# Performance work log

Measured on AMD Instinct MI355X. Metric: run time of the kernel, lower is better.

## Reference

```python
import jax, jax.numpy as jnp
import numpy as np

IN_NC = 32
OUT_NC = 32
HIDDEN = 192  # in_nc * expand_ratio(6)
KS = 3
EPS = 1e-5


def setup_inputs() -> dict:
    key = jax.random.key(0)
    k1, k2 = jax.random.split(key)
    b, h, w = 8, 128, 128
    fh = fw = 8
    hyper = IN_NC * HIDDEN + HIDDEN * KS * KS + HIDDEN * OUT_NC  # 14016
    return {
        "x": jax.random.normal(k1, (b, IN_NC, h, w), jnp.float32),
        "s": jax.random.normal(k2, (b, hyper, fh, fw), jnp.float32),
        "g1": jnp.ones((HIDDEN,), jnp.float32),
        "b1": jnp.zeros((HIDDEN,), jnp.float32),
        "g2": jnp.ones((HIDDEN,), jnp.float32),
        "b2": jnp.zeros((HIDDEN,), jnp.float32),
        "g3": jnp.ones((OUT_NC,), jnp.float32),
        "b3": jnp.zeros((OUT_NC,), jnp.float32),
    }


def _bn(x, gamma, beta):
    # x: [P, H, W, C]; training-mode BatchNorm2d over (P, H, W) per channel
    mean = jnp.mean(x, axis=(0, 1, 2))
    var = jnp.var(x, axis=(0, 1, 2))  # biased, matches torch normalization
    return (x - mean) * jax.lax.rsqrt(var + EPS) * gamma + beta


def _relu6(x):
    return jnp.clip(x, 0.0, 6.0)


def _forward(x, s, g1, b1, g2, b2, g3, b3):
    b, c, h, w = x.shape
    fh, fw = s.shape[-2], s.shape[-1]
    ph, pw = h // fh, w // fw
    kh, kw = ph + 2, pw + 2  # padding (1,1)

    # reflect-pad then unfold into per-patch tiles [P, kh, kw, c]
    xp = jnp.pad(x, ((0, 0), (0, 0), (1, 1), (1, 1)), mode="reflect")
    xp = xp.transpose(0, 2, 3, 1)  # [b, h+2, w+2, c]
    ih = jnp.arange(fh)[:, None] * ph + jnp.arange(kh)[None, :]  # [fh, kh]
    iw = jnp.arange(fw)[:, None] * pw + jnp.arange(kw)[None, :]  # [fw, kw]
    t = xp[:, ih]            # [b, fh, kh, w+2, c]
    t = t[:, :, :, iw]       # [b, fh, kh, fw, kw, c]
    patches = t.transpose(0, 1, 3, 2, 4, 5).reshape(b * fh * fw, kh, kw, c)

    # per-patch hypernet weights
    wt = s.transpose(0, 2, 3, 1).reshape(b * fh * fw, -1)  # [P, hyper]
    r1 = IN_NC * HIDDEN
    r2 = r1 + HIDDEN * KS * KS
    w1 = wt[:, :r1].reshape(-1, HIDDEN, IN_NC)          # pointwise expand
    w2 = wt[:, r1:r2].reshape(-1, HIDDEN, KS, KS)        # depthwise 3x3
    w3 = wt[:, r2:].reshape(-1, OUT_NC, HIDDEN)          # pointwise project

    # 1x1 expand + BN + ReLU6
    x1 = jnp.einsum("pijc,poc->pijo", patches, w1)       # [P, kh, kw, hidden]
    x1 = _relu6(_bn(x1, g1, b1))

    # depthwise 3x3 (valid, stride 1) + BN + ReLU6
    ii = jnp.arange(ph)[:, None] + jnp.arange(KS)[None, :]
    jj = jnp.arange(pw)[:, None] + jnp.arange(KS)[None, :]
    win = x1[:, ii]          # [P, ph, 3, kw, hidden]
    win = win[:, :, :, jj]   # [P, ph, 3, pw, 3, hidden]
    x2 = jnp.einsum("piujvc,pcuv->pijc", win, w2)        # [P, ph, pw, hidden]
    x2 = _relu6(_bn(x2, g2, b2))

    # 1x1 project + BN
    x3 = jnp.einsum("pijc,poc->pijo", x2, w3)            # [P, ph, pw, out]
    x3 = _bn(x3, g3, b3)

    out = x3.reshape(b, fh, fw, ph, pw, OUT_NC)
    out = out.transpose(0, 5, 1, 3, 2, 4).reshape(b, OUT_NC, h, w)
    return x + out  # use_res_connect: stride==1 and in_nc==out_nc


def reference(x, s, g1, b1, g2, b2, g3, b3):
    return _forward(x, s, g1, b1, g2, b2, g3, b3)
```

## Files before the change

kernel.cpp:

```cpp
#include <hip/hip_runtime.h>

#define EPS 1e-5f

namespace {
constexpr int HYPER = 14016;
constexpr int HID   = 192;
constexpr int A1    = 324;
constexpr int A2    = 256;
constexpr int P_TOT = 512;
constexpr int W1SZ  = 6144;
constexpr int WT2SZ = 7872;
constexpr int R3OFF = 1728;

constexpr size_t WB1_B = 0;
constexpr size_t WT2_B = 6291456;
constexpr size_t X2_B  = WT2_B + 16121856;
constexpr size_t X3_B  = X2_B + 50331648;
constexpr size_t SUM_B = X3_B + 16777216;
}

typedef __attribute__((ext_vector_type(8))) short bf16x8;
typedef __attribute__((ext_vector_type(4))) float f32x4;

__device__ __forceinline__ float relu6f(float v) { return fminf(fmaxf(v, 0.f), 6.f); }

__device__ __forceinline__ float bf2f(unsigned int h) {
  return __uint_as_float(h << 16);
}
__device__ __forceinline__ unsigned short f2bf(float f) {
  unsigned int u = __float_as_uint(f);
  return (unsigned short)((u + 0x7FFFu + ((u >> 16) & 1u)) >> 16);
}

__device__ __host__ __forceinline__ int afrag_slot(int o, int c) {
  return (o >> 4) * 512 + (c >> 3) * 128 + (o & 15) * 8 + (c & 7);
}

__global__ __launch_bounds__(256) void k0_transpose(const float* __restrict__ s,
                                                    unsigned short* __restrict__ wb1,
                                                    float* __restrict__ wt2) {
  __shared__ float tile[64][65];
  const int blk = blockIdx.x;
  const int b  = blk / 219;
  const int kt = blk - b * 219;
  const int k0 = kt * 64;
  const int t  = threadIdx.x;
  {
    const int f  = t & 63;
    const int kr = t >> 6;
    const float* sp = s + ((size_t)b * HYPER + k0 + kr) * 64 + f;
#pragma unroll
    for (int kk = 0; kk < 16; kk++)
      tile[kr + kk * 4][f] = sp[(size_t)kk * 4 * 64];
  }
  __syncthreads();
  {
    const int kk = t & 63;
    const int fr = t >> 6;
    if (kt < 96) {
      const int k = k0 + kk;
      const int o = k >> 5, c = k & 31;
      const int slot = afrag_slot(o, c);
      unsigned short* wp = wb1 + ((size_t)b * 64 + fr) * W1SZ + slot;
#pragma unroll
      for (int ff = 0; ff < 16; ff++)
        wp[(size_t)ff * 4 * W1SZ] = f2bf(tile[kk][fr + ff * 4]);
    } else {
      float* wp = wt2 + ((size_t)b * 64 + fr) * WT2SZ + (k0 - W1SZ) + kk;
#pragma unroll
      for (int ff = 0; ff < 16; ff++)
        wp[(size_t)ff * 4 * WT2SZ] = tile[kk][fr + ff * 4];
    }
  }
}

__global__ __launch_bounds__(256) void k1_stats(const float* __restrict__ x,
                                                const unsigned short* __restrict__ wb1,
                                                float* __restrict__ sums) {
  __shared__ __align__(16) unsigned short pL[21 * 512];
  __shared__ float stat[384];
  const int p  = blockIdx.x;
  const int b  = p >> 6;
  const int fi = (p >> 3) & 7;
  const int fj = p & 7;
  const int t  = threadIdx.x;

  for (int i = t; i < 384; i += 256) stat[i] = 0.f;

  const int row0 = fi * 16 - 1, col0 = fj * 16 - 1;
  const float* xb = x + (size_t)b * 32 * 128 * 128;
  for (int idx = t; idx < 32 * A1; idx += 256) {
    int c  = idx / A1;
    int ij = idx - c * A1;
    int ii = ij / 18;
    int jj = ij - ii * 18;
    int r  = row0 + ii; r  = (r  < 0) ? 1 : (r  > 127) ? 126 : r;
    int cl = col0 + jj; cl = (cl < 0) ? 1 : (cl > 127) ? 126 : cl;
    int slot = ((ij >> 4) * 4 + (c >> 3)) * 128 + (ij & 15) * 8 + (c & 7);
    pL[slot] = f2bf(xb[((size_t)c * 128 + r) * 128 + cl]);
  }
  __syncthreads();

  const int lane = t & 63;
  const int wv   = t >> 6;
  const int m16  = lane & 15;
  const int quad = lane >> 4;
  const unsigned short* wbp = wb1 + (size_t)p * W1SZ;

  for (int oi = 0; oi < 3; oi++) {
    const int ot = wv + oi * 4;
    bf16x8 a = *(const bf16x8*)(wbp + ot * 512 + lane * 8);
    float sacc[4] = {0.f, 0.f, 0.f, 0.f};
    float qacc[4] = {0.f, 0.f, 0.f, 0.f};
    for (int jt = 0; jt < 21; jt++) {
      bf16x8 bb = *(const bf16x8*)&pL[jt * 512 + lane * 8];
      f32x4 d = __builtin_amdgcn_mfma_f32_16x16x32_bf16(a, bb, (f32x4){0.f, 0.f, 0.f, 0.f}, 0, 0, 0);
      const int ij = jt * 16 + m16;
      if (ij < A1) {
#pragma unroll
        for (int r = 0; r < 4; r++) {
          float v = d[r];
          sacc[r] += v;
          qacc[r] = fmaf(v, v, qacc[r]);
        }
      }
    }
#pragma unroll
    for (int r = 0; r < 4; r++) {
      float sv = sacc[r], qv = qacc[r];
#pragma unroll
      for (int msk = 1; msk < 16; msk <<= 1) {
        sv += __shfl_xor(sv, msk, 64);
        qv += __shfl_xor(qv, msk, 64);
      }
      if (m16 == 0) {
        int o = ot * 16 + quad * 4 + r;
        atomicAdd(&stat[o], sv);
        atomicAdd(&stat[192 + o], qv);
      }
    }
  }
  __syncthreads();
  for (int i = t; i < 384; i += 256) atomicAdd(&sums[i], stat[i]);
}

__global__ __launch_bounds__(256) void k2_fused(const float* __restrict__ x,
                                                const unsigned short* __restrict__ wb1,
                                                const float* __restrict__ wt2,
                                                const float* __restrict__ sums,
                                                const float* __restrict__ g1,
                                                const float* __restrict__ b1,
                                                unsigned short* __restrict__ x2,
                                                float* __restrict__ sums2) {
  __shared__ __align__(16) unsigned short pL[21 * 512];
  __shared__ __align__(16) unsigned short xc[2][324 * 18];
  __shared__ __align__(16) unsigned short x2s[256 * 18];
  __shared__ float sc[HID], sh[HID];
  __shared__ float st2[384];
  const int p  = blockIdx.x;
  const int b  = p >> 6;
  const int fi = (p >> 3) & 7;
  const int fj = p & 7;
  const int t  = threadIdx.x;

  const float inv1 = 1.f / 165888.f;
  for (int c = t; c < HID; c += 256) {
    float m   = sums[c] * inv1;
    float var = sums[192 + c] * inv1 - m * m;
    float scl = g1[c] * rsqrtf(var + EPS);
    sc[c] = scl;
    sh[c] = b1[c] - m * scl;
  }
  for (int i = t; i < 384; i += 256) st2[i] = 0.f;

  const int row0 = fi * 16 - 1, col0 = fj * 16 - 1;
  const float* xb = x + (size_t)b * 32 * 128 * 128;
  for (int idx = t; idx < 32 * A1; idx += 256) {
    int c  = idx / A1;
    int ij = idx - c * A1;
    int ii = ij / 18;
    int jj = ij - ii * 18;
    int r  = row0 + ii; r  = (r  < 0) ? 1 : (r  > 127) ? 126 : r;
    int cl = col0 + jj; cl = (cl < 0) ? 1 : (cl > 127) ? 126 : cl;
    int slot = ((ij >> 4) * 4 + (c >> 3)) * 128 + (ij & 15) * 8 + (c & 7);
    pL[slot] = f2bf(xb[((size_t)c * 128 + r) * 128 + cl]);
  }
  __syncthreads();

  const int lane = t & 63;
  const int wv   = t >> 6;
  const int m16  = lane & 15;
  const int quad = lane >> 4;
  const int cdw  = t >> 4;
  const int jdw  = t & 15;
  const float* w2p = wt2 + (size_t)p * WT2SZ;
  unsigned short* x2base = x2 + (size_t)p * 12 * 4096;
  const unsigned short* wbp = wb1 + (size_t)p * W1SZ;

  for (int ri = 0; ri < 6; ri++) {
    const int sub = wv & 1;
    const int ot  = ri * 2 + sub;
    const int jt0 = (wv >> 1) * 11;
    const int jt1 = jt0 + 11 - (wv >> 1);
    bf16x8 a = *(const bf16x8*)(wbp + ot * 512 + lane * 8);
    for (int jt = jt0; jt < jt1; jt++) {
      bf16x8 bb = *(const bf16x8*)&pL[jt * 512 + lane * 8];
      f32x4 d = __builtin_amdgcn_mfma_f32_16x16x32_bf16(a, bb, (f32x4){0.f, 0.f, 0.f, 0.f}, 0, 0, 0);
      const int ij = jt * 16 + m16;
      if (ij < A1) {
        unsigned short* xcp = &xc[sub][ij * 18 + quad * 4];
#pragma unroll
        for (int r = 0; r < 4; r++) {
          int ch = ot * 16 + quad * 4 + r;
          float v = relu6f(fmaf(d[r], sc[ch], sh[ch]));
          xcp[r] = f2bf(v);
        }
      }
    }
    __syncthreads();
    for (int sub2 = 0; sub2 < 2; sub2++) {
      const int ot2 = ri * 2 + sub2;
      const int ch  = ot2 * 16 + cdw;
      float wr[9];
#pragma unroll
      for (int u = 0; u < 9; u++) wr[u] = w2p[ch * 9 + u];
      float accs[16];
#pragma unroll
      for (int i = 0; i < 16; i++) accs[i] = 0.f;
      const unsigned short* xcs = &xc[sub2][0];
#pragma unroll
      for (int r = 0; r < 18; r++) {
        const unsigned short* bp = &xcs[(r * 18 + jdw) * 18 + cdw];
        float v0 = bf2f(bp[0]);
        float v1 = bf2f(bp[18]);
        float v2 = bf2f(bp[36]);
#pragma unroll
        for (int u = 0; u < 3; u++) {
          int i = r - u;
          if (i >= 0 && i < 16)
            accs[i] = fmaf(v0, wr[u * 3 + 0],
                      fmaf(v1, wr[u * 3 + 1],
                      fmaf(v2, wr[u * 3 + 2], accs[i])));
        }
      }
      float ls = 0.f, lq = 0.f;
#pragma unroll
      for (int i = 0; i < 16; i++) {
        unsigned short h = f2bf(accs[i]);
        float rv = bf2f(h);
        ls += rv;
        lq = fmaf(rv, rv, lq);
        x2s[(i * 16 + jdw) * 18 + cdw] = h;
      }
#pragma unroll
      for (int msk = 1; msk < 16; msk <<= 1) {
        ls += __shfl_xor(ls, msk, 64);
        lq += __shfl_xor(lq, msk, 64);
      }
      if (jdw == 0) {
        atomicAdd(&st2[ch], ls);
        atomicAdd(&st2[192 + ch], lq);
      }
      __syncthreads();
      unsigned short* dst = x2base + (size_t)ot2 * 4096;
#pragma unroll
      for (int k = 0; k < 4; k++) {
        int g  = (k * 256 + t) * 4;
        int ij = g >> 4, c0 = g & 15;
        unsigned int a0 = *(const unsigned int*)&x2s[ij * 18 + c0];
        unsigned int a1 = *(const unsigned int*)&x2s[ij * 18 + c0 + 2];
        uint2 v; v.x = a0; v.y = a1;
        *(uint2*)&dst[g] = v;
      }
      __syncthreads();
    }
  }
  for (int i = t; i < 384; i += 256) atomicAdd(&sums2[i], st2[i]);
}

__global__ __launch_bounds__(256) void k3_pw2(const unsigned short* __restrict__ x2,
                                              const float* __restrict__ wt2,
                                              const float* __restrict__ sums2,
                                              const float* __restrict__ g2,
                                              const float* __restrict__ b2,
                                              float* __restrict__ x3,
                                              float* __restrict__ sums3) {
  __shared__ __align__(16) unsigned short wA[12 * 512];
  __shared__ float sc[HID], sh[HID];
  __shared__ float st3[64];
  const int blk  = blockIdx.x;
  const int p    = blk >> 1;
  const int half = blk & 1;
  const int t    = threadIdx.x;
  const float inv = 1.f / 131072.f;
  for (int c = t; c < HID; c += 256) {
    float m   = sums2[c] * inv;
    float var = sums2[192 + c] * inv - m * m;
    float scl = g2[c] * rsqrtf(var + EPS);
    sc[c] = scl;
    sh[c] = b2[c] - m * scl;
  }
  if (t < 64) st3[t] = 0.f;
  const float* w3p = wt2 + (size_t)p * WT2SZ + R3OFF;
  for (int idx = t; idx < 32 * 48; idx += 256) {
    int o  = idx / 48;
    int c4 = idx - o * 48;
    float4 v = *(const float4*)&w3p[o * HID + c4 * 4];
    int slot = ((o >> 4) * 6 + (c4 >> 3)) * 512 + ((((c4 >> 1) & 3) * 16) + (o & 15)) * 8 + (c4 & 1) * 4;
    ushort4 u;
    u.x = f2bf(v.x); u.y = f2bf(v.y); u.z = f2bf(v.z); u.w = f2bf(v.w);
    *(ushort4*)&wA[slot] = u;
  }
  __syncthreads();
  const int lane = t & 63;
  const int wv   = t >> 6;
  const int m16  = lane & 15;
  const int kg   = lane >> 4;
  bf16x8 aF[2][6];
#pragma unroll
  for (int ot = 0; ot < 2; ot++)
#pragma unroll
    for (int ks = 0; ks < 6; ks++)
      aF[ot][ks] = *(const bf16x8*)&wA[(ot * 6 + ks) * 512 + lane * 8];
  const unsigned short* x2p = x2 + (size_t)p * 12 * 4096;
  f32x4 acc[2][2];
#pragma unroll
  for (int it = 0; it < 2; it++)
#pragma unroll
    for (int ot = 0; ot < 2; ot++)
#pragma unroll
      for (int r = 0; r < 4; r++) acc[it][ot][r] = 0.f;
#pragma unroll
  for (int it = 0; it < 2; it++) {
    const int ijt = half * 8 + wv + it * 4;
    const int ij  = ijt * 16 + m16;
    const unsigned short* brow = x2p + (size_t)(kg >> 1) * 4096 + (size_t)ij * 16 + (kg & 1) * 8;
#pragma unroll
    for (int ks = 0; ks < 6; ks++) {
      ushort4 u0 = *(const ushort4*)&brow[ks * 8192];
      ushort4 u1 = *(const ushort4*)&brow[ks * 8192 + 4];
      const float* scp = &sc[ks * 32 + kg * 8];
      const float* shp = &sh[ks * 32 + kg * 8];
      unsigned short uu[8] = {u0.x, u0.y, u0.z, u0.w, u1.x, u1.y, u1.z, u1.w};
      bf16x8 bb;
#pragma unroll
      for (int j = 0; j < 8; j++) {
        float y = relu6f(fmaf(bf2f(uu[j]), scp[j], shp[j]));
        bb[j] = (short)f2bf(y);
      }
      acc[it][0] = __builtin_amdgcn_mfma_f32_16x16x32_bf16(aF[0][ks], bb, acc[it][0], 0, 0, 0);
      acc[it][1] = __builtin_amdgcn_mfma_f32_16x16x32_bf16(aF[1][ks], bb, acc[it][1], 0, 0, 0);
    }
  }
  float* x3p = x3 + (size_t)p * 32 * A2;
  float sacc[2][4] = {{0.f}}, qacc[2][4] = {{0.f}};
#pragma unroll
  for (int it = 0; it < 2; it++) {
    const int ijt = half * 8 + wv + it * 4;
#pragma unroll
    for (int ot = 0; ot < 2; ot++) {
#pragma unroll
      for (int r = 0; r < 4; r++) {
        float v = acc[it][ot][r];
        x3p[(size_t)(ot * 16 + kg * 4 + r) * A2 + ijt * 16 + m16] = v;
        sacc[ot][r] += v;
        qacc[ot][r] = fmaf(v, v, qacc[ot][r]);
      }
    }
  }
#pragma unroll
  for (int ot = 0; ot < 2; ot++)
#pragma unroll
    for (int r = 0; r < 4; r++) {
      float sv = sacc[ot][r], qv = qacc[ot][r];
#pragma unroll
      for (int msk = 1; msk < 16; msk <<= 1) {
        sv += __shfl_xor(sv, msk, 64);
        qv += __shfl_xor(qv, msk, 64);
      }
      if (m16 == 0) {
        int o = ot * 16 + kg * 4 + r;
        atomicAdd(&st3[o], sv);
        atomicAdd(&st3[32 + o], qv);
      }
    }
  __syncthreads();
  if (t < 64) atomicAdd(&sums3[t], st3[t]);
}

__global__ __launch_bounds__(256) void k4_out(const float* __restrict__ x,
                                              const float* __restrict__ x3,
                                              const float* __restrict__ sums3,
                                              const float* __restrict__ g3,
                                              const float* __restrict__ b3,
                                              float* __restrict__ out) {
  const int idx4 = blockIdx.x * 256 + threadIdx.x;
  const int w4 = idx4 & 31;
  int tmp = idx4 >> 5;
  const int h = tmp & 127; tmp >>= 7;
  const int o = tmp & 31;
  const int b = tmp >> 5;
  const int fi = h >> 4, i = h & 15;
  const int fj = w4 >> 2;
  const int j0 = (w4 & 3) * 4;
  const int p   = b * 64 + fi * 8 + fj;
  const int ij0 = i * 16 + j0;
  const float inv = 1.f / 131072.f;
  float m   = sums3[o] * inv;
  float var = sums3[32 + o] * inv - m * m;
  float sv  = g3[o] * rsqrtf(var + EPS);
  float shv = b3[o] - m * sv;
  float4 xv = *(const float4*)&x[(size_t)idx4 * 4];
  float4 v  = *(const float4*)&x3[((size_t)p * 32 + o) * A2 + ij0];
  float4 r;
  r.x = fmaf(v.x, sv, shv) + xv.x;
  r.y = fmaf(v.y, sv, shv) + xv.y;
  r.z = fmaf(v.z, sv, shv) + xv.z;
  r.w = fmaf(v.w, sv, shv) + xv.w;
  *(float4*)&out[(size_t)idx4 * 4] = r;
}

extern "C" void kernel_launch(void* const* d_in, const int* in_sizes, int n_in,
                              void* d_out, int out_size, void* d_ws, size_t ws_size,
                              hipStream_t stream) {
  const float* x  = (const float*)d_in[0];
  const float* s  = (const float*)d_in[1];
  const float* g1 = (const float*)d_in[2];
  const float* b1 = (const float*)d_in[3];
  const float* g2 = (const float*)d_in[4];
  const float* b2 = (const float*)d_in[5];
  const float* g3 = (const float*)d_in[6];
  const float* b3 = (const float*)d_in[7];
  char* base = (char*)d_ws;
  unsigned short* wb1  = (unsigned short*)(base + WB1_B);
  float*          wt2  = (float*)(base + WT2_B);
  unsigned short* x2   = (unsigned short*)(base + X2_B);
  float*          x3   = (float*)(base + X3_B);
  float*          sums = (float*)(base + SUM_B);
  float* out = (float*)d_out;

  hipMemsetAsync(sums, 0, 832 * sizeof(float), stream);
  k0_transpose<<<8 * 219, 256, 0, stream>>>(s, wb1, wt2);
  k1_stats<<<P_TOT, 256, 0, stream>>>(x, wb1, sums);
  k2_fused<<<P_TOT, 256, 0, stream>>>(x, wb1, wt2, sums, g1, b1, x2, sums + 384);
  k3_pw2<<<1024, 256, 0, stream>>>(x2, wt2, sums + 384, g2, b2, x3, sums + 768);
  k4_out<<<4096, 256, 0, stream>>>(x, x3, sums + 768, g3, b3, out);
}
```

Measured before the change: 223.0 us.

## Restructure fused depthwise stage and store projection output as bf16

The fused expand+depthwise kernel now processes one 16-channel tile at a time. It interleaves the next tile's MFMA expand with the current tile's store, stages the depthwise weights in shared memory, and switches to a channel-major xc layout where each thread computes two adjacent columns over eight rows. The projection output x3 is stored as bf16 rather than fp32, which halves the intermediate traffic between k3 and k4, and the BN statistics are taken on the rounded values. This trades some accuracy in the final BN input for less memory traffic, and cuts the barriers per channel group in k2.

New measurement: 221.0 us. About the same (-0.9%).

```diff
diff --git a/kernel.cpp b/kernel.cpp
--- a/kernel.cpp
+++ b/kernel.cpp
@@ -16,7 +16,7 @@
 constexpr size_t WT2_B = 6291456;
 constexpr size_t X2_B  = WT2_B + 16121856;
 constexpr size_t X3_B  = X2_B + 50331648;
-constexpr size_t SUM_B = X3_B + 16777216;
+constexpr size_t SUM_B = X3_B + 8388608;
 }
 
 typedef __attribute__((ext_vector_type(8))) short bf16x8;
@@ -153,8 +153,9 @@
                                                 unsigned short* __restrict__ x2,
                                                 float* __restrict__ sums2) {
   __shared__ __align__(16) unsigned short pL[21 * 512];
-  __shared__ __align__(16) unsigned short xc[2][324 * 18];
+  __shared__ __align__(16) unsigned short xc[16 * 328];
   __shared__ __align__(16) unsigned short x2s[256 * 18];
+  __shared__ float w2L[HID * 9];
   __shared__ float sc[HID], sh[HID];
   __shared__ float st2[384];
   const int p  = blockIdx.x;
@@ -172,6 +173,10 @@
     sh[c] = b1[c] - m * scl;
   }
   for (int i = t; i < 384; i += 256) st2[i] = 0.f;
+  {
+    const float* wtp = wt2 + (size_t)p * WT2SZ;
+    for (int i = t; i < HID * 9; i += 256) w2L[i] = wtp[i];
+  }
 
   const int row0 = fi * 16 - 1, col0 = fj * 16 - 1;
   const float* xb = x + (size_t)b * 32 * 128 * 128;
@@ -191,89 +196,95 @@
   const int wv   = t >> 6;
   const int m16  = lane & 15;
   const int quad = lane >> 4;
-  const int cdw  = t >> 4;
-  const int jdw  = t & 15;
-  const float* w2p = wt2 + (size_t)p * WT2SZ;
+  const int ih  = t >> 7;
+  const int cdw = (t >> 3) & 15;
+  const int jp  = t & 7;
+  const unsigned short* wbp = wb1 + (size_t)p * W1SZ;
   unsigned short* x2base = x2 + (size_t)p * 12 * 4096;
-  const unsigned short* wbp = wb1 + (size_t)p * W1SZ;
-
-  for (int ri = 0; ri < 6; ri++) {
-    const int sub = wv & 1;
-    const int ot  = ri * 2 + sub;
-    const int jt0 = (wv >> 1) * 11;
-    const int jt1 = jt0 + 11 - (wv >> 1);
-    bf16x8 a = *(const bf16x8*)(wbp + ot * 512 + lane * 8);
-    for (int jt = jt0; jt < jt1; jt++) {
+
+  auto conv1 = [&](int rt) {
+    bf16x8 a = *(const bf16x8*)(wbp + rt * 512 + lane * 8);
+    for (int jt = wv; jt < 21; jt += 4) {
       bf16x8 bb = *(const bf16x8*)&pL[jt * 512 + lane * 8];
       f32x4 d = __builtin_amdgcn_mfma_f32_16x16x32_bf16(a, bb, (f32x4){0.f, 0.f, 0.f, 0.f}, 0, 0, 0);
       const int ij = jt * 16 + m16;
       if (ij < A1) {
-        unsigned short* xcp = &xc[sub][ij * 18 + quad * 4];
 #pragma unroll
         for (int r = 0; r < 4; r++) {
-          int ch = ot * 16 + quad * 4 + r;
+          int cl = quad * 4 + r;
+          int ch = rt * 16 + cl;
           float v = relu6f(fmaf(d[r], sc[ch], sh[ch]));
-          xcp[r] = f2bf(v);
+          xc[cl * 328 + ij] = f2bf(v);
         }
       }
     }
-    __syncthreads();
-    for (int sub2 = 0; sub2 < 2; sub2++) {
-      const int ot2 = ri * 2 + sub2;
-      const int ch  = ot2 * 16 + cdw;
+  };
+
+  conv1(0);
+  __syncthreads();
+
+  for (int rt = 0; rt < 12; rt++) {
+    {
+      const int ch = rt * 16 + cdw;
       float wr[9];
 #pragma unroll
-      for (int u = 0; u < 9; u++) wr[u] = w2p[ch * 9 + u];
-      float accs[16];
-#pragma unroll
-      for (int i = 0; i < 16; i++) accs[i] = 0.f;
-      const unsigned short* xcs = &xc[sub2][0];
-#pragma unroll
-      for (int r = 0; r < 18; r++) {
-        const unsigned short* bp = &xcs[(r * 18 + jdw) * 18 + cdw];
-        float v0 = bf2f(bp[0]);
-        float v1 = bf2f(bp[18]);
-        float v2 = bf2f(bp[36]);
+      for (int u = 0; u < 9; u++) wr[u] = w2L[ch * 9 + u];
+      float a0[8], a1[8];
+#pragma unroll
+      for (int i = 0; i < 8; i++) { a0[i] = 0.f; a1[i] = 0.f; }
+      const unsigned short* xcc = &xc[cdw * 328];
+#pragma unroll
+      for (int rr = 0; rr < 10; rr++) {
+        const int rg = ih * 8 + rr;
+        unsigned int d0 = *(const unsigned int*)&xcc[rg * 18 + jp * 2];
+        unsigned int d1 = *(const unsigned int*)&xcc[rg * 18 + jp * 2 + 2];
+        float v0 = bf2f(d0 & 0xFFFFu), v1 = bf2f(d0 >> 16);
+        float v2 = bf2f(d1 & 0xFFFFu), v3 = bf2f(d1 >> 16);
 #pragma unroll
         for (int u = 0; u < 3; u++) {
-          int i = r - u;
-          if (i >= 0 && i < 16)
-            accs[i] = fmaf(v0, wr[u * 3 + 0],
-                      fmaf(v1, wr[u * 3 + 1],
-                      fmaf(v2, wr[u * 3 + 2], accs[i])));
+          int il = rr - u;
+          if (il >= 0 && il < 8) {
+            a0[il] = fmaf(v0, wr[u * 3 + 0], fmaf(v1, wr[u * 3 + 1], fmaf(v2, wr[u * 3 + 2], a0[il])));
+            a1[il] = fmaf(v1, wr[u * 3 + 0], fmaf(v2, wr[u * 3 + 1], fmaf(v3, wr[u * 3 + 2], a1[il])));
+          }
         }
       }
       float ls = 0.f, lq = 0.f;
 #pragma unroll
-      for (int i = 0; i < 16; i++) {
-        unsigned short h = f2bf(accs[i]);
-        float rv = bf2f(h);
-        ls += rv;
-        lq = fmaf(rv, rv, lq);
-        x2s[(i * 16 + jdw) * 18 + cdw] = h;
-      }
-#pragma unroll
-      for (int msk = 1; msk < 16; msk <<= 1) {
-        ls += __shfl_xor(ls, msk, 64);
-        lq += __shfl_xor(lq, msk, 64);
-      }
-      if (jdw == 0) {
+      for (int il = 0; il < 8; il++) {
+        const int ig = ih * 8 + il;
+        const int j0 = jp * 2;
+        unsigned short h0 = f2bf(a0[il]);
+        unsigned short h1 = f2bf(a1[il]);
+        float r0 = bf2f(h0), r1 = bf2f(h1);
+        ls += r0 + r1;
+        lq = fmaf(r0, r0, fmaf(r1, r1, lq));
+        x2s[(ig * 16 + j0) * 18 + cdw]     = h0;
+        x2s[(ig * 16 + j0 + 1) * 18 + cdw] = h1;
+      }
+      ls += __shfl_xor(ls, 1, 64); lq += __shfl_xor(lq, 1, 64);
+      ls += __shfl_xor(ls, 2, 64); lq += __shfl_xor(lq, 2, 64);
+      ls += __shfl_xor(ls, 4, 64); lq += __shfl_xor(lq, 4, 64);
+      if (jp == 0) {
         atomicAdd(&st2[ch], ls);
         atomicAdd(&st2[192 + ch], lq);
       }
-      __syncthreads();
-      unsigned short* dst = x2base + (size_t)ot2 * 4096;
+    }
+    __syncthreads();
+    {
+      unsigned short* dst = x2base + (size_t)rt * 4096;
 #pragma unroll
       for (int k = 0; k < 4; k++) {
         int g  = (k * 256 + t) * 4;
         int ij = g >> 4, c0 = g & 15;
-        unsigned int a0 = *(const unsigned int*)&x2s[ij * 18 + c0];
-        unsigned int a1 = *(const unsigned int*)&x2s[ij * 18 + c0 + 2];
-        uint2 v; v.x = a0; v.y = a1;
+        unsigned int v0 = *(const unsigned int*)&x2s[ij * 18 + c0];
+        unsigned int v1 = *(const unsigned int*)&x2s[ij * 18 + c0 + 2];
+        uint2 v; v.x = v0; v.y = v1;
         *(uint2*)&dst[g] = v;
       }
-      __syncthreads();
-    }
+    }
+    if (rt < 11) conv1(rt + 1);
+    __syncthreads();
   }
   for (int i = t; i < 384; i += 256) atomicAdd(&sums2[i], st2[i]);
 }
@@ -283,7 +294,7 @@
                                               const float* __restrict__ sums2,
                                               const float* __restrict__ g2,
                                               const float* __restrict__ b2,
-                                              float* __restrict__ x3,
+                                              unsigned short* __restrict__ x3,
                                               float* __restrict__ sums3) {
   __shared__ __align__(16) unsigned short wA[12 * 512];
   __shared__ float sc[HID], sh[HID];
@@ -352,7 +363,7 @@
       acc[it][1] = __builtin_amdgcn_mfma_f32_16x16x32_bf16(aF[1][ks], bb, acc[it][1], 0, 0, 0);
     }
   }
-  float* x3p = x3 + (size_t)p * 32 * A2;
+  unsigned short* x3p = x3 + (size_t)p * 32 * A2;
   float sacc[2][4] = {{0.f}}, qacc[2][4] = {{0.f}};
 #pragma unroll
   for (int it = 0; it < 2; it++) {
@@ -361,8 +372,9 @@
     for (int ot = 0; ot < 2; ot++) {
 #pragma unroll
       for (int r = 0; r < 4; r++) {
-        float v = acc[it][ot][r];
-        x3p[(size_t)(ot * 16 + kg * 4 + r) * A2 + ijt * 16 + m16] = v;
+        unsigned short h = f2bf(acc[it][ot][r]);
+        float v = bf2f(h);
+        x3p[(size_t)(ot * 16 + kg * 4 + r) * A2 + ijt * 16 + m16] = h;
         sacc[ot][r] += v;
         qacc[ot][r] = fmaf(v, v, qacc[ot][r]);
       }
@@ -389,7 +401,7 @@
 }
 
 __global__ __launch_bounds__(256) void k4_out(const float* __restrict__ x,
-                                              const float* __restrict__ x3,
+                                              const unsigned short* __restrict__ x3,
                                               const float* __restrict__ sums3,
                                               const float* __restrict__ g3,
                                               const float* __restrict__ b3,
@@ -411,12 +423,12 @@
   float sv  = g3[o] * rsqrtf(var + EPS);
   float shv = b3[o] - m * sv;
   float4 xv = *(const float4*)&x[(size_t)idx4 * 4];
-  float4 v  = *(const float4*)&x3[((size_t)p * 32 + o) * A2 + ij0];
+  ushort4 u = *(const ushort4*)&x3[((size_t)p * 32 + o) * A2 + ij0];
   float4 r;
-  r.x = fmaf(v.x, sv, shv) + xv.x;
-  r.y = fmaf(v.y, sv, shv) + xv.y;
-  r.z = fmaf(v.z, sv, shv) + xv.z;
-  r.w = fmaf(v.w, sv, shv) + xv.w;
+  r.x = fmaf(bf2f(u.x), sv, shv) + xv.x;
+  r.y = fmaf(bf2f(u.y), sv, shv) + xv.y;
+  r.z = fmaf(bf2f(u.z), sv, shv) + xv.z;
+  r.w = fmaf(bf2f(u.w), sv, shv) + xv.w;
   *(float4*)&out[(size_t)idx4 * 4] = r;
 }
 
@@ -435,7 +447,7 @@
   unsigned short* wb1  = (unsigned short*)(base + WB1_B);
   float*          wt2  = (float*)(base + WT2_B);
   unsigned short* x2   = (unsigned short*)(base + X2_B);
-  float*          x3   = (float*)(base + X3_B);
+  unsigned short* x3   = (unsigned short*)(base + X3_B);
   float*          sums = (float*)(base + SUM_B);
   float* out = (float*)d_out;
 
```
